# Performance work log

Hardware: AMD Instinct MI355X
Metric: run time of the kernel (lower is better)

The kernel has to match this reference:

```python
import jax, jax.numpy as jnp
import numpy as np

C = 1.0          # curvature of PoincareBall
SQRT_C = 1.0
MIN_NORM = 1e-15
PROJ_EPS = 4e-3  # float32 boundary eps used by PoincareBall.proj
N_NODES = 50000


def _norm(x):
    return jnp.clip(jnp.linalg.norm(x, axis=-1, keepdims=True), MIN_NORM)


def _artanh(x):
    return jnp.arctanh(jnp.clip(x, -1.0 + 1e-7, 1.0 - 1e-7))


def proj(x):
    # clip points to the open ball of radius (1-eps)/sqrt(c)
    norm = _norm(x)
    maxnorm = (1.0 - PROJ_EPS) / SQRT_C
    return jnp.where(norm > maxnorm, x / norm * maxnorm, x)


def expmap0(u):
    u_norm = _norm(u)
    return jnp.tanh(SQRT_C * u_norm) * u / (SQRT_C * u_norm)


def logmap0(p):
    p_norm = _norm(p)
    return _artanh(SQRT_C * p_norm) * p / (SQRT_C * p_norm)


def mobius_add(x, y):
    x2 = jnp.sum(x * x, -1, keepdims=True)
    y2 = jnp.sum(y * y, -1, keepdims=True)
    xy = jnp.sum(x * y, -1, keepdims=True)
    num = (1.0 + 2.0 * C * xy + C * y2) * x + (1.0 - C * x2) * y
    den = 1.0 + 2.0 * C * xy + C * C * x2 * y2
    return num / jnp.clip(den, MIN_NORM)


def mobius_matvec(m, x):
    x_norm = _norm(x)
    mx = x @ m.T  # [N, d_out]
    mx_norm = _norm(mx)
    res = jnp.tanh(mx_norm / x_norm * _artanh(SQRT_C * x_norm)) * mx / (mx_norm * SQRT_C)
    zero_row = jnp.all(mx == 0, axis=-1, keepdims=True)
    return jnp.where(zero_row, jnp.zeros_like(res), res)


def setup_inputs() -> dict:
    key = jax.random.key(0)
    k = jax.random.split(key, 6)
    n, d_in, d_out, n_edges = N_NODES, 256, 96, 800000
    # points on the Poincare ball
    x = proj(0.02 * jax.random.normal(k[0], (n, d_in), jnp.float32))
    weight = jax.random.normal(k[1], (d_out, d_in), jnp.float32) * (1.0 / np.sqrt(d_in)).astype(np.float32)
    bias = jax.random.normal(k[2], (d_out,), jnp.float32) * 0.01
    edge_row = jax.random.randint(k[3], (n_edges,), 0, n)
    edge_col = jax.random.randint(k[4], (n_edges,), 0, n)
    # normalized adjacency weights ~ 1/avg_degree
    edge_weight = jax.random.uniform(k[5], (n_edges,), jnp.float32) * (1.0 / 16.0)
    return {"x": x, "weight": weight, "bias": bias, "edge_weight": edge_weight,
            "edge_row": edge_row, "edge_col": edge_col}


def reference(x, weight, bias, edge_weight, edge_row, edge_col):
    # --- HypLinear (dropout inactive in eval) ---
    h = proj(mobius_matvec(weight, x))
    hyp_bias = proj(expmap0(bias[None, :]))  # proj_tan0 is identity on the ball
    h = proj(mobius_add(h, hyp_bias))
    # --- HypAgg: spmm(adj, logmap0(h)) then expmap0 ---
    xt = logmap0(h)                                  # [N, d_out]
    msgs = edge_weight[:, None] * xt[edge_col]       # [E, d_out]
    support = jax.ops.segment_sum(msgs, edge_row, num_segments=N_NODES)
    h = proj(expmap0(support))
    # --- HypAct: relu in tangent space, map back (c_in == c_out) ---
    h = proj(expmap0(jax.nn.relu(logmap0(h))))
    return h
```

## Files before the change

### kernel.cpp

```cpp
#include <hip/hip_runtime.h>


typedef __attribute__((ext_vector_type(8))) short short8;
typedef __attribute__((ext_vector_type(4))) float floatx4;

#define DIN 256
#define DOUT 96
#define MAXN 0.996f
#define EPS15 1e-15f
#define ATC (1.0f - 1e-7f)
#define STR 48

__device__ __forceinline__ float us2f(unsigned short u) {
    unsigned int v = ((unsigned int)u) << 16;
    return __uint_as_float(v);
}
__device__ __forceinline__ unsigned short f2us(float f) {
    unsigned int b = __float_as_uint(f);
    unsigned int r = (b + 0x7FFFu + ((b >> 16) & 1u)) >> 16;
    return (unsigned short)r;
}

__global__ void initzero_kernel(const unsigned short* __restrict__ xraw,
                                const void* __restrict__ bias,
                                const void* __restrict__ wgt,
                                float* __restrict__ ws,
                                int* __restrict__ deg, int N) {
    int i = blockIdx.x * blockDim.x + threadIdx.x;
    int stride = gridDim.x * blockDim.x;
    for (int k = i; k < N; k += stride) deg[k] = 0;

    if (blockIdx.x == 0 && threadIdx.x < 64) {
        int l = threadIdx.x;
        float v0 = us2f(xraw[l]);
        float v1 = us2f(xraw[64 + l]);
        int big = (!(fabsf(v0) < 1e4f)) || (!(fabsf(v1) < 1e4f));
        #pragma unroll
        for (int m = 32; m >= 1; m >>= 1) big |= __shfl_xor(big, m, 64);
        bool isb = !big;
        if (l == 0) ws[97] = isb ? 1.0f : 0.0f;

        float b0 = isb ? us2f(((const unsigned short*)bias)[l])
                       : ((const float*)bias)[l];
        float b1 = 0.0f;
        if (l < 32)
            b1 = isb ? us2f(((const unsigned short*)bias)[64 + l])
                     : ((const float*)bias)[64 + l];
        float n2 = b0 * b0 + b1 * b1;
        #pragma unroll
        for (int m = 32; m >= 1; m >>= 1) n2 += __shfl_xor(n2, m, 64);
        float bn = fmaxf(sqrtf(n2), EPS15);
        float ef = tanhf(bn) / bn;
        float hn = ef * sqrtf(n2);
        float s = (hn > MAXN) ? MAXN / fmaxf(hn, EPS15) : 1.0f;
        ws[l] = s * ef * b0;
        if (l < 32) ws[64 + l] = s * ef * b1;
        if (l == 0) { float v = s * hn; ws[96] = v * v; }
    }

    if (blockIdx.x == 1) {
        int t = threadIdx.x, lane = t & 63;
        float v0 = us2f(xraw[lane]);
        float v1 = us2f(xraw[64 + lane]);
        int big = (!(fabsf(v0) < 1e4f)) || (!(fabsf(v1) < 1e4f));
        #pragma unroll
        for (int m = 32; m >= 1; m >>= 1) big |= __shfl_xor(big, m, 64);
        bool isb = !big;
        uint4* wz = (uint4*)(ws + 128);
        if (isb) {
            const uint4* wg = (const uint4*)wgt;
            #pragma unroll
            for (int it = 0; it < 12; it++) {
                int g = t + 256 * it;
                int c = g >> 5, j = g & 31;
                int f = c >> 4, mr = c & 15;
                int kt = j >> 2, q = j & 3;
                wz[(f * 8 + kt) * 64 + q * 16 + mr] = wg[g];
            }
        } else {
            const float* wgf = (const float*)wgt;
            #pragma unroll
            for (int it = 0; it < 12; it++) {
                int g = t + 256 * it;
                int c = g >> 5, j = g & 31;
                int f = c >> 4, mr = c & 15;
                int kt = j >> 2, q = j & 3;
                const float* src = wgf + (size_t)c * DIN + j * 8;
                unsigned short tmp[8];
                #pragma unroll
                for (int z = 0; z < 8; z++) tmp[z] = f2us(src[z]);
                wz[(f * 8 + kt) * 64 + q * 16 + mr] = *(const uint4*)tmp;
            }
        }
    }
}

__global__ void fillhyp_kernel(const void* __restrict__ x,
                               const void* __restrict__ ew,
                               const int* __restrict__ erow,
                               const int* __restrict__ ecol,
                               float* __restrict__ ws,
                               unsigned int* __restrict__ einfo,
                               unsigned short* __restrict__ xtb,
                               int* __restrict__ deg,
                               int N, int E, int Fb) {
    const int t = threadIdx.x;
    const bool isb = ws[97] != 0.0f;

    int b = blockIdx.x;
    bool isfill; int idx;
    if (b < 2 * Fb) { isfill = (b & 1); idx = b >> 1; }
    else            { isfill = false;   idx = b - Fb; }

    if (isfill) {
        int stride = Fb * 256;
        for (int e = idx * 256 + t; e < E; e += stride) {
            unsigned int wbits = isb ? (unsigned int)((const unsigned short*)ew)[e]
                                     : (unsigned int)f2us(((const float*)ew)[e]);
            int row = erow[e];
            int p = atomicAdd(&deg[row], 1);
            if (p < STR)
                einfo[(size_t)row * STR + p] = (wbits << 16) | (unsigned int)ecol[e];
        }
        return;
    }

    const int lane = t & 63;
    const int wv = t >> 6;
    const int mrow = lane & 15;
    const int quad = lane >> 4;
    const uint4* __restrict__ Wg = (const uint4*)(ws + 128);

    const int r0 = (idx * 4 + wv) * 16;
    if (r0 >= N) return;

    float hbl[6];
    #pragma unroll
    for (int f = 0; f < 6; f++) hbl[f] = ws[mrow + 16 * f];
    const float hb2 = ws[96];

    int xr = r0 + mrow; if (xr >= N) xr = N - 1;
    short8 afrag[8];
    if (isb) {
        const unsigned short* xrow = (const unsigned short*)x + (size_t)xr * DIN + quad * 8;
        #pragma unroll
        for (int kt = 0; kt < 8; kt++)
            afrag[kt] = *(const short8*)(xrow + kt * 32);
    } else {
        const float* xrow = (const float*)x + (size_t)xr * DIN + quad * 8;
        #pragma unroll
        for (int kt = 0; kt < 8; kt++) {
            short8 a;
            #pragma unroll
            for (int j = 0; j < 8; j++) a[j] = (short)f2us(xrow[kt * 32 + j]);
            afrag[kt] = a;
        }
    }

    float xn2p = 0.f;
    #pragma unroll
    for (int kt = 0; kt < 8; kt++)
        #pragma unroll
        for (int j = 0; j < 8; j++) {
            float v = us2f((unsigned short)afrag[kt][j]);
            xn2p = fmaf(v, v, xn2p);
        }
    xn2p += __shfl_xor(xn2p, 16, 64);
    xn2p += __shfl_xor(xn2p, 32, 64);

    floatx4 acc[6];
    #pragma unroll
    for (int f = 0; f < 6; f++) acc[f] = (floatx4){0.f, 0.f, 0.f, 0.f};
    #pragma unroll
    for (int f = 0; f < 6; f++) {
        uint4 bw[8];
        #pragma unroll
        for (int kt = 0; kt < 8; kt++)
            bw[kt] = Wg[(f * 8 + kt) * 64 + lane];
        #pragma unroll
        for (int kt = 0; kt < 8; kt++) {
            short8 bfr = *(const short8*)&bw[kt];
            acc[f] = __builtin_amdgcn_mfma_f32_16x16x32_bf16(afrag[kt], bfr, acc[f], 0, 0, 0);
        }
    }

    float mxn2[4], dmh[4];
    #pragma unroll
    for (int reg = 0; reg < 4; reg++) {
        float a2 = 0.f, ad = 0.f;
        #pragma unroll
        for (int f = 0; f < 6; f++) {
            float v = acc[f][reg];
            a2 = fmaf(v, v, a2);
            ad = fmaf(v, hbl[f], ad);
        }
        mxn2[reg] = a2; dmh[reg] = ad;
    }
    #pragma unroll
    for (int m = 8; m >= 1; m >>= 1)
        #pragma unroll
        for (int reg = 0; reg < 4; reg++) {
            mxn2[reg] += __shfl_xor(mxn2[reg], m, 64);
            dmh[reg]  += __shfl_xor(dmh[reg],  m, 64);
        }

    int sel = mrow & 3;
    float xn2  = __shfl(xn2p, quad * 4 + sel, 64);
    float wmx2 = mxn2[sel], wdmh = dmh[sel];

    float xn  = fmaxf(sqrtf(xn2), EPS15);
    float mxn = fmaxf(sqrtf(wmx2), EPS15);
    float g   = (mxn / xn) * atanhf(fminf(xn, ATC));
    float tg  = tanhf(g);
    float rs0 = tg / mxn;
    float rn  = rs0 * sqrtf(wmx2);
    float s1  = (rn > MAXN) ? MAXN / fmaxf(rn, EPS15) : 1.0f;
    float al  = s1 * rs0;
    float x2  = al * al * wmx2;
    float xy  = al * wdmh;
    float cA  = 1.0f + 2.0f * xy + hb2;
    float cB  = 1.0f - x2;
    float den = fmaxf(1.0f + 2.0f * xy + x2 * hb2, EPS15);
    float p   = cA * al / den;
    float qq  = cB / den;
    float o2  = p*p*wmx2 + 2.0f*p*qq*wdmh + qq*qq*hb2;
    float on  = sqrtf(fmaxf(o2, 0.0f));
    float s2  = (on > MAXN) ? MAXN / fmaxf(on, EPS15) : 1.0f;
    float pn  = fmaxf(s2 * on, EPS15);
    float F   = (atanhf(fminf(pn, ATC)) / pn) * s2;
    float Fp_m = F * p, Fq_m = F * qq;

    float Fp[4], Fq[4];
    #pragma unroll
    for (int reg = 0; reg < 4; reg++) {
        Fp[reg] = __shfl(Fp_m, quad * 16 + reg, 64);
        Fq[reg] = __shfl(Fq_m, quad * 16 + reg, 64);
    }

    #pragma unroll
    for (int reg = 0; reg < 4; reg++) {
        int row = r0 + quad * 4 + reg;
        if (row < N) {
            size_t base = (size_t)row * DOUT + mrow;
            #pragma unroll
            for (int f = 0; f < 6; f++)
                xtb[base + 16 * f] = f2us(fmaf(Fp[reg], acc[f][reg], Fq[reg] * hbl[f]));
        }
    }
}

__global__ void agg_kernel(const unsigned short* __restrict__ xtb,
                           const unsigned int* __restrict__ einfo,
                           const int* __restrict__ deg,
                           float* __restrict__ ws,
                           void* __restrict__ out, int N) {
    int wv = threadIdx.x >> 6, lane = threadIdx.x & 63;
    int node = blockIdx.x * 4 + wv;
    if (node >= N) return;
    const bool isb = ws[97] != 0.0f;
    const bool act = lane < 48;

    int cnt = deg[node]; if (cnt > STR) cnt = STR;
    size_t base = (size_t)node * STR;
    float acc0 = 0.f, acc1 = 0.f;

    unsigned int my = (lane < cnt) ? einfo[base + lane] : 0u;

    int j = 0;
    for (; j + 8 <= cnt; j += 8) {
        float w[8]; const unsigned int* sp[8];
        #pragma unroll
        for (int k = 0; k < 8; k++) {
            unsigned int ei = (unsigned int)__shfl((int)my, j + k, 64);
            w[k] = __uint_as_float(ei & 0xFFFF0000u);
            sp[k] = (const unsigned int*)(xtb + (size_t)(ei & 0xFFFFu) * DOUT);
        }
        unsigned int u[8];
        #pragma unroll
        for (int k = 0; k < 8; k++) u[k] = act ? sp[k][lane] : 0u;
        #pragma unroll
        for (int k = 0; k < 8; k++) {
            acc0 = fmaf(w[k], __uint_as_float(u[k] << 16), acc0);
            acc1 = fmaf(w[k], __uint_as_float(u[k] & 0xFFFF0000u), acc1);
        }
    }
    for (; j < cnt; j++) {
        unsigned int ei = (unsigned int)__shfl((int)my, j, 64);
        float w = __uint_as_float(ei & 0xFFFF0000u);
        unsigned int u = act
            ? ((const unsigned int*)(xtb + (size_t)(ei & 0xFFFFu) * DOUT))[lane] : 0u;
        acc0 = fmaf(w, __uint_as_float(u << 16), acc0);
        acc1 = fmaf(w, __uint_as_float(u & 0xFFFF0000u), acc1);
    }

    float u0 = acc0, u1 = acc1;
    float n2 = u0*u0 + u1*u1;
    #pragma unroll
    for (int m = 32; m >= 1; m >>= 1) n2 += __shfl_xor(n2, m, 64);
    float un = fmaxf(sqrtf(n2), EPS15);
    float ef = tanhf(un) / un;
    float p0 = ef * u0, p1 = ef * u1;
    float pnrm = ef * sqrtf(n2);
    float sc = (pnrm > MAXN) ? MAXN / fmaxf(pnrm, EPS15) : 1.0f;
    p0 *= sc; p1 *= sc; pnrm *= sc;
    float pncl = fmaxf(pnrm, EPS15);
    float lf = atanhf(fminf(pncl, ATC)) / pncl;
    float t0 = fmaxf(lf * p0, 0.0f), t1 = fmaxf(lf * p1, 0.0f);
    float tn2 = t0*t0 + t1*t1;
    #pragma unroll
    for (int m = 32; m >= 1; m >>= 1) tn2 += __shfl_xor(tn2, m, 64);
    float tn = fmaxf(sqrtf(tn2), EPS15);
    float ef2 = tanhf(tn) / tn;
    float en = ef2 * sqrtf(tn2);
    float s2 = (en > MAXN) ? MAXN / fmaxf(en, EPS15) : 1.0f;
    float scale = s2 * ef2;
    float v0 = scale * t0, v1 = scale * t1;

    if (act) {
        if (isb) {
            unsigned int pk = ((unsigned int)f2us(v1) << 16) | (unsigned int)f2us(v0);
            ((unsigned int*)((unsigned short*)out + (size_t)node * DOUT))[lane] = pk;
        } else {
            float2 fv; fv.x = v0; fv.y = v1;
            ((float2*)((float*)out + (size_t)node * DOUT))[lane] = fv;
        }
    }
}

extern "C" void kernel_launch(void* const* d_in, const int* in_sizes, int n_in,
                              void* d_out, int out_size, void* d_ws, size_t ws_size,
                              hipStream_t stream) {
    const void* x    = d_in[0];
    const void* wgt  = d_in[1];
    const void* bias = d_in[2];
    const void* ew   = d_in[3];
    const int* erow  = (const int*)d_in[4];
    const int* ecol  = (const int*)d_in[5];

    int N = out_size / DOUT;
    int E = in_sizes[4];
    size_t nd = (size_t)N * DOUT;

    float* wsf = (float*)d_ws;
    unsigned int* einfo = (unsigned int*)(wsf + 128 + 12288);
    unsigned short* xtb = (unsigned short*)(einfo + (size_t)N * STR);
    int* deg            = (int*)(xtb + nd);

    int Hb = (N + 63) / 64;
    int Fb = (Hb + 1) / 2;

    initzero_kernel<<<128, 256, 0, stream>>>((const unsigned short*)x, bias, wgt, wsf, deg, N);
    fillhyp_kernel<<<Hb + Fb, 256, 0, stream>>>(x, ew, erow, ecol, wsf,
                                                einfo, xtb, deg, N, E, Fb);
    agg_kernel<<<(N + 3) / 4, 256, 0, stream>>>(xtb, einfo, deg, wsf, d_out, N);
}
```

Baseline: 190.7 us.

## Pad degree counters, batch fill atomics, double-buffer gathers, parallelize weight repack

Degree counters are spread to one per 64-byte stride when workspace allows, to cut atomic contention and false sharing between rows. The edge-fill loop now handles four edges per thread, issuing all loads before the atomics so more memory requests are in flight. The aggregation gather is double-buffered so the next 8 neighbor loads are issued before the current batch is accumulated. Weight repacking is split across 12 blocks instead of one. The padded counters raise zero-init traffic and workspace use, and the unrolled aggregation raises register pressure.

```diff
diff --git a/kernel.cpp b/kernel.cpp
--- a/kernel.cpp
+++ b/kernel.cpp
@@ -25,10 +25,11 @@
                                 const void* __restrict__ bias,
                                 const void* __restrict__ wgt,
                                 float* __restrict__ ws,
-                                int* __restrict__ deg, int N) {
+                                int* __restrict__ deg, int N, int dstr) {
     int i = blockIdx.x * blockDim.x + threadIdx.x;
     int stride = gridDim.x * blockDim.x;
-    for (int k = i; k < N; k += stride) deg[k] = 0;
+    int tot = N * dstr;
+    for (int k = i; k < tot; k += stride) deg[k] = 0;
 
     if (blockIdx.x == 0 && threadIdx.x < 64) {
         int l = threadIdx.x;
@@ -58,7 +59,7 @@
         if (l == 0) { float v = s * hn; ws[96] = v * v; }
     }
 
-    if (blockIdx.x == 1) {
+    if (blockIdx.x >= 1 && blockIdx.x <= 12) {
         int t = threadIdx.x, lane = t & 63;
         float v0 = us2f(xraw[lane]);
         float v1 = us2f(xraw[64 + lane]);
@@ -67,30 +68,20 @@
         for (int m = 32; m >= 1; m >>= 1) big |= __shfl_xor(big, m, 64);
         bool isb = !big;
         uint4* wz = (uint4*)(ws + 128);
+        int g = t + 256 * (int)(blockIdx.x - 1);
+        int c = g >> 5, j = g & 31;
+        int f = c >> 4, mr = c & 15;
+        int kt = j >> 2, q = j & 3;
         if (isb) {
             const uint4* wg = (const uint4*)wgt;
-            #pragma unroll
-            for (int it = 0; it < 12; it++) {
-                int g = t + 256 * it;
-                int c = g >> 5, j = g & 31;
-                int f = c >> 4, mr = c & 15;
-                int kt = j >> 2, q = j & 3;
-                wz[(f * 8 + kt) * 64 + q * 16 + mr] = wg[g];
-            }
+            wz[(f * 8 + kt) * 64 + q * 16 + mr] = wg[g];
         } else {
             const float* wgf = (const float*)wgt;
-            #pragma unroll
-            for (int it = 0; it < 12; it++) {
-                int g = t + 256 * it;
-                int c = g >> 5, j = g & 31;
-                int f = c >> 4, mr = c & 15;
-                int kt = j >> 2, q = j & 3;
-                const float* src = wgf + (size_t)c * DIN + j * 8;
-                unsigned short tmp[8];
-                #pragma unroll
-                for (int z = 0; z < 8; z++) tmp[z] = f2us(src[z]);
-                wz[(f * 8 + kt) * 64 + q * 16 + mr] = *(const uint4*)tmp;
-            }
+            const float* src = wgf + (size_t)c * DIN + j * 8;
+            unsigned short tmp[8];
+            #pragma unroll
+            for (int z = 0; z < 8; z++) tmp[z] = f2us(src[z]);
+            wz[(f * 8 + kt) * 64 + q * 16 + mr] = *(const uint4*)tmp;
         }
     }
 }
@@ -103,7 +94,7 @@
                                unsigned int* __restrict__ einfo,
                                unsigned short* __restrict__ xtb,
                                int* __restrict__ deg,
-                               int N, int E, int Fb) {
+                               int N, int E, int Fb, int dstr) {
     const int t = threadIdx.x;
     const bool isb = ws[97] != 0.0f;
 
@@ -113,14 +104,29 @@
     else            { isfill = false;   idx = b - Fb; }
 
     if (isfill) {
-        int stride = Fb * 256;
-        for (int e = idx * 256 + t; e < E; e += stride) {
-            unsigned int wbits = isb ? (unsigned int)((const unsigned short*)ew)[e]
-                                     : (unsigned int)f2us(((const float*)ew)[e]);
-            int row = erow[e];
-            int p = atomicAdd(&deg[row], 1);
-            if (p < STR)
-                einfo[(size_t)row * STR + p] = (wbits << 16) | (unsigned int)ecol[e];
+        const int T4 = Fb * 1024;
+        for (int e0 = idx * 1024 + t; e0 < E; e0 += T4) {
+            int row[4], col[4]; unsigned int wb[4]; bool va[4];
+            #pragma unroll
+            for (int u = 0; u < 4; u++) {
+                int e = e0 + 256 * u;
+                va[u] = e < E;
+                if (va[u]) {
+                    wb[u] = isb ? (unsigned int)((const unsigned short*)ew)[e]
+                                : (unsigned int)f2us(((const float*)ew)[e]);
+                    row[u] = erow[e];
+                    col[u] = ecol[e];
+                }
+            }
+            int p[4];
+            #pragma unroll
+            for (int u = 0; u < 4; u++)
+                if (va[u]) p[u] = atomicAdd(&deg[row[u] * dstr], 1);
+            #pragma unroll
+            for (int u = 0; u < 4; u++)
+                if (va[u] && p[u] < STR)
+                    einfo[(size_t)row[u] * STR + p[u]] =
+                        (wb[u] << 16) | (unsigned int)col[u];
         }
         return;
     }
@@ -253,45 +259,63 @@
                            const unsigned int* __restrict__ einfo,
                            const int* __restrict__ deg,
                            float* __restrict__ ws,
-                           void* __restrict__ out, int N) {
+                           void* __restrict__ out, int N, int dstr) {
     int wv = threadIdx.x >> 6, lane = threadIdx.x & 63;
     int node = blockIdx.x * 4 + wv;
     if (node >= N) return;
     const bool isb = ws[97] != 0.0f;
     const bool act = lane < 48;
 
-    int cnt = deg[node]; if (cnt > STR) cnt = STR;
+    int cnt = deg[(size_t)node * dstr]; if (cnt > STR) cnt = STR;
     size_t base = (size_t)node * STR;
     float acc0 = 0.f, acc1 = 0.f;
 
     unsigned int my = (lane < cnt) ? einfo[base + lane] : 0u;
 
-    int j = 0;
-    for (; j + 8 <= cnt; j += 8) {
-        float w[8]; const unsigned int* sp[8];
-        #pragma unroll
-        for (int k = 0; k < 8; k++) {
-            unsigned int ei = (unsigned int)__shfl((int)my, j + k, 64);
-            w[k] = __uint_as_float(ei & 0xFFFF0000u);
-            sp[k] = (const unsigned int*)(xtb + (size_t)(ei & 0xFFFFu) * DOUT);
-        }
-        unsigned int u[8];
-        #pragma unroll
-        for (int k = 0; k < 8; k++) u[k] = act ? sp[k][lane] : 0u;
-        #pragma unroll
-        for (int k = 0; k < 8; k++) {
-            acc0 = fmaf(w[k], __uint_as_float(u[k] << 16), acc0);
-            acc1 = fmaf(w[k], __uint_as_float(u[k] & 0xFFFF0000u), acc1);
-        }
-    }
-    for (; j < cnt; j++) {
-        unsigned int ei = (unsigned int)__shfl((int)my, j, 64);
-        float w = __uint_as_float(ei & 0xFFFF0000u);
-        unsigned int u = act
-            ? ((const unsigned int*)(xtb + (size_t)(ei & 0xFFFFu) * DOUT))[lane] : 0u;
-        acc0 = fmaf(w, __uint_as_float(u << 16), acc0);
-        acc1 = fmaf(w, __uint_as_float(u & 0xFFFF0000u), acc1);
-    }
+    unsigned int uA[8], uB[8];
+    float wA[8], wB[8];
+
+#define ISSUE(BU, BW, B)                                                       \
+    _Pragma("unroll")                                                          \
+    for (int k = 0; k < 8; k++) {                                              \
+        unsigned int ei = (unsigned int)__shfl((int)my, (B) * 8 + k, 64);      \
+        BW[k] = __uint_as_float(ei & 0xFFFF0000u);                             \
+        const unsigned int* sp =                                               \
+            (const unsigned int*)(xtb + (size_t)(ei & 0xFFFFu) * DOUT);        \
+        BU[k] = (act && ((B) * 8 + k) < cnt) ? sp[lane] : 0u;                  \
+    }
+
+#define CONSUME(BU, BW)                                                        \
+    _Pragma("unroll")                                                          \
+    for (int k = 0; k < 8; k++) {                                              \
+        acc0 = fmaf(BW[k], __uint_as_float(BU[k] << 16), acc0);                \
+        acc1 = fmaf(BW[k], __uint_as_float(BU[k] & 0xFFFF0000u), acc1);        \
+    }
+
+    if (cnt > 0) {
+        ISSUE(uA, wA, 0);
+        if (cnt > 8) ISSUE(uB, wB, 1);
+        CONSUME(uA, wA);
+        if (cnt > 8) {
+            if (cnt > 16) ISSUE(uA, wA, 2);
+            CONSUME(uB, wB);
+            if (cnt > 16) {
+                if (cnt > 24) ISSUE(uB, wB, 3);
+                CONSUME(uA, wA);
+                if (cnt > 24) {
+                    if (cnt > 32) ISSUE(uA, wA, 4);
+                    CONSUME(uB, wB);
+                    if (cnt > 32) {
+                        if (cnt > 40) ISSUE(uB, wB, 5);
+                        CONSUME(uA, wA);
+                        if (cnt > 40) CONSUME(uB, wB);
+                    }
+                }
+            }
+        }
+    }
+#undef ISSUE
+#undef CONSUME
 
     float u0 = acc0, u1 = acc1;
     float n2 = u0*u0 + u1*u1;
@@ -346,11 +370,14 @@
     unsigned short* xtb = (unsigned short*)(einfo + (size_t)N * STR);
     int* deg            = (int*)(xtb + nd);
 
+    size_t fixed_bytes = ((size_t)(128 + 12288) + (size_t)N * STR) * 4 + nd * 2;
+    int dstr = (ws_size >= fixed_bytes + (size_t)N * 16 * 4) ? 16 : 1;
+
     int Hb = (N + 63) / 64;
     int Fb = (Hb + 1) / 2;
 
-    initzero_kernel<<<128, 256, 0, stream>>>((const unsigned short*)x, bias, wgt, wsf, deg, N);
+    initzero_kernel<<<128, 256, 0, stream>>>((const unsigned short*)x, bias, wgt, wsf, deg, N, dstr);
     fillhyp_kernel<<<Hb + Fb, 256, 0, stream>>>(x, ew, erow, ecol, wsf,
-                                                einfo, xtb, deg, N, E, Fb);
-    agg_kernel<<<(N + 3) / 4, 256, 0, stream>>>(xtb, einfo, deg, wsf, d_out, N);
-}
+                                                einfo, xtb, deg, N, E, Fb, dstr);
+    agg_kernel<<<(N + 3) / 4, 256, 0, stream>>>(xtb, einfo, deg, wsf, d_out, N, dstr);
+}
```

After: 182.2 us. -4.5%, faster.

## Replace per-node atomic edge lists with block-bucketed partition and LDS-atomic aggregation

Applied to the files above, without the earlier changes.

Edges are now bucketed by row block (128 rows per bucket) through a tiled partition kernel. It builds a local histogram and prefix sum in shared memory, then reserves one global atomic per bucket, which replaces the per-edge global atomics on node degree counters. Aggregation runs one block per bucket and accumulates messages into a 128x96 shared-memory tile with LDS atomics, using double-buffered gathers. The hyperbolic linear stage is split into its own kernel, and the weight repacking is spread over 12 blocks. This changes the per-node cap of 48 edges to a per-bucket cap of 2560 and hardcodes the bucket count to the problem size. It also adds heavy shared-atomic contention and low parallelism in aggregation, since there are only 391 blocks.

```diff
diff --git a/kernel.cpp b/kernel.cpp
--- a/kernel.cpp
+++ b/kernel.cpp
@@ -9,7 +9,9 @@
 #define MAXN 0.996f
 #define EPS15 1e-15f
 #define ATC (1.0f - 1e-7f)
-#define STR 48
+#define NBK 391
+#define CAP 2560
+#define TILE 6144
 
 __device__ __forceinline__ float us2f(unsigned short u) {
     unsigned int v = ((unsigned int)u) << 16;
@@ -25,10 +27,10 @@
                                 const void* __restrict__ bias,
                                 const void* __restrict__ wgt,
                                 float* __restrict__ ws,
-                                int* __restrict__ deg, int N) {
+                                int* __restrict__ gcur) {
     int i = blockIdx.x * blockDim.x + threadIdx.x;
     int stride = gridDim.x * blockDim.x;
-    for (int k = i; k < N; k += stride) deg[k] = 0;
+    for (int k = i; k < NBK * 16; k += stride) gcur[k] = 0;
 
     if (blockIdx.x == 0 && threadIdx.x < 64) {
         int l = threadIdx.x;
@@ -58,7 +60,7 @@
         if (l == 0) { float v = s * hn; ws[96] = v * v; }
     }
 
-    if (blockIdx.x == 1) {
+    if (blockIdx.x >= 1 && blockIdx.x <= 12) {
         int t = threadIdx.x, lane = t & 63;
         float v0 = us2f(xraw[lane]);
         float v1 = us2f(xraw[64 + lane]);
@@ -67,71 +69,115 @@
         for (int m = 32; m >= 1; m >>= 1) big |= __shfl_xor(big, m, 64);
         bool isb = !big;
         uint4* wz = (uint4*)(ws + 128);
+        int g = t + 256 * (int)(blockIdx.x - 1);
+        int c = g >> 5, j = g & 31;
+        int f = c >> 4, mr = c & 15;
+        int kt = j >> 2, q = j & 3;
         if (isb) {
             const uint4* wg = (const uint4*)wgt;
-            #pragma unroll
-            for (int it = 0; it < 12; it++) {
-                int g = t + 256 * it;
-                int c = g >> 5, j = g & 31;
-                int f = c >> 4, mr = c & 15;
-                int kt = j >> 2, q = j & 3;
-                wz[(f * 8 + kt) * 64 + q * 16 + mr] = wg[g];
-            }
+            wz[(f * 8 + kt) * 64 + q * 16 + mr] = wg[g];
         } else {
             const float* wgf = (const float*)wgt;
+            const float* src = wgf + (size_t)c * DIN + j * 8;
+            unsigned short tmp[8];
             #pragma unroll
-            for (int it = 0; it < 12; it++) {
-                int g = t + 256 * it;
-                int c = g >> 5, j = g & 31;
-                int f = c >> 4, mr = c & 15;
-                int kt = j >> 2, q = j & 3;
-                const float* src = wgf + (size_t)c * DIN + j * 8;
-                unsigned short tmp[8];
-                #pragma unroll
-                for (int z = 0; z < 8; z++) tmp[z] = f2us(src[z]);
-                wz[(f * 8 + kt) * 64 + q * 16 + mr] = *(const uint4*)tmp;
-            }
-        }
-    }
-}
-
-__global__ void fillhyp_kernel(const void* __restrict__ x,
-                               const void* __restrict__ ew,
-                               const int* __restrict__ erow,
-                               const int* __restrict__ ecol,
-                               float* __restrict__ ws,
-                               unsigned int* __restrict__ einfo,
-                               unsigned short* __restrict__ xtb,
-                               int* __restrict__ deg,
-                               int N, int E, int Fb) {
+            for (int z = 0; z < 8; z++) tmp[z] = f2us(src[z]);
+            wz[(f * 8 + kt) * 64 + q * 16 + mr] = *(const uint4*)tmp;
+        }
+    }
+}
+
+__global__ void __launch_bounds__(256) part_kernel(
+        const void* __restrict__ ew,
+        const int* __restrict__ erow,
+        const int* __restrict__ ecol,
+        const float* __restrict__ ws,
+        int* __restrict__ gcur,
+        uint2* __restrict__ arena, int E) {
+    __shared__ uint2 stage[TILE];
+    __shared__ int h[NBK], excl[NBK], cur[NBK], gb[NBK];
+    __shared__ int cb[64];
+
     const int t = threadIdx.x;
     const bool isb = ws[97] != 0.0f;
-
-    int b = blockIdx.x;
-    bool isfill; int idx;
-    if (b < 2 * Fb) { isfill = (b & 1); idx = b >> 1; }
-    else            { isfill = false;   idx = b - Fb; }
-
-    if (isfill) {
-        int stride = Fb * 256;
-        for (int e = idx * 256 + t; e < E; e += stride) {
-            unsigned int wbits = isb ? (unsigned int)((const unsigned short*)ew)[e]
-                                     : (unsigned int)f2us(((const float*)ew)[e]);
-            int row = erow[e];
-            int p = atomicAdd(&deg[row], 1);
-            if (p < STR)
-                einfo[(size_t)row * STR + p] = (wbits << 16) | (unsigned int)ecol[e];
-        }
-        return;
-    }
-
+    const int tb = blockIdx.x * TILE;
+    const int tcnt = min(TILE, E - tb);
+
+    for (int i = t; i < NBK; i += 256) h[i] = 0;
+    __syncthreads();
+
+    int rw[24]; unsigned int pk[24];
+    #pragma unroll
+    for (int k = 0; k < 24; k++) {
+        int e = tb + t + 256 * k;
+        if (e < E) {
+            int r = erow[e];
+            unsigned int wb = isb ? (unsigned int)((const unsigned short*)ew)[e]
+                                  : (unsigned int)f2us(((const float*)ew)[e]);
+            rw[k] = r;
+            pk[k] = (wb << 16) | (unsigned int)ecol[e];
+            atomicAdd(&h[r >> 7], 1);
+        } else rw[k] = -1;
+    }
+    __syncthreads();
+
+    if (t < 64) {
+        int s = 0;
+        #pragma unroll
+        for (int j = 0; j < 8; j++) {
+            int b2 = t * 8 + j;
+            if (b2 < NBK) s += h[b2];
+        }
+        int sc = s;
+        #pragma unroll
+        for (int d = 1; d < 64; d <<= 1) {
+            int tt = __shfl_up(sc, d, 64);
+            if (t >= d) sc += tt;
+        }
+        cb[t] = sc - s;
+    }
+    __syncthreads();
+    for (int b2 = t; b2 < NBK; b2 += 256) {
+        int base = cb[b2 >> 3];
+        int x = 0;
+        for (int j = (b2 & ~7); j < b2; j++) x += h[j];
+        excl[b2] = base + x;
+        cur[b2]  = base + x;
+        gb[b2] = atomicAdd(&gcur[b2 * 16], h[b2]);
+    }
+    __syncthreads();
+
+    #pragma unroll
+    for (int k = 0; k < 24; k++) {
+        if (rw[k] >= 0) {
+            int b2 = rw[k] >> 7;
+            int slot = atomicAdd(&cur[b2], 1);
+            stage[slot] = make_uint2(pk[k], (unsigned int)rw[k]);
+        }
+    }
+    __syncthreads();
+
+    for (int s = t; s < tcnt; s += 256) {
+        uint2 ent = stage[s];
+        int b2 = (int)ent.y >> 7;
+        int p = gb[b2] + (s - excl[b2]);
+        if (p < CAP) arena[(size_t)b2 * CAP + p] = ent;
+    }
+}
+
+__global__ void hyp_kernel(const void* __restrict__ x,
+                           float* __restrict__ ws,
+                           unsigned short* __restrict__ xtb,
+                           int N) {
+    const int t = threadIdx.x;
+    const bool isb = ws[97] != 0.0f;
     const int lane = t & 63;
     const int wv = t >> 6;
     const int mrow = lane & 15;
     const int quad = lane >> 4;
     const uint4* __restrict__ Wg = (const uint4*)(ws + 128);
 
-    const int r0 = (idx * 4 + wv) * 16;
+    const int r0 = ((int)blockIdx.x * 4 + wv) * 16;
     if (r0 >= N) return;
 
     float hbl[6];
@@ -249,80 +295,109 @@
     }
 }
 
-__global__ void agg_kernel(const unsigned short* __restrict__ xtb,
-                           const unsigned int* __restrict__ einfo,
-                           const int* __restrict__ deg,
-                           float* __restrict__ ws,
-                           void* __restrict__ out, int N) {
-    int wv = threadIdx.x >> 6, lane = threadIdx.x & 63;
-    int node = blockIdx.x * 4 + wv;
-    if (node >= N) return;
+__global__ void __launch_bounds__(512) agg_kernel(
+        const unsigned short* __restrict__ xtb,
+        const uint2* __restrict__ arena,
+        const int* __restrict__ gcur,
+        const float* __restrict__ ws,
+        void* __restrict__ out, int N) {
+    __shared__ float acc[128 * 96];
+
+    const int t = threadIdx.x;
+    const int lane = t & 63, wv = t >> 6;
+    const int b = blockIdx.x;
     const bool isb = ws[97] != 0.0f;
-    const bool act = lane < 48;
-
-    int cnt = deg[node]; if (cnt > STR) cnt = STR;
-    size_t base = (size_t)node * STR;
-    float acc0 = 0.f, acc1 = 0.f;
-
-    unsigned int my = (lane < cnt) ? einfo[base + lane] : 0u;
-
-    int j = 0;
-    for (; j + 8 <= cnt; j += 8) {
-        float w[8]; const unsigned int* sp[8];
-        #pragma unroll
-        for (int k = 0; k < 8; k++) {
-            unsigned int ei = (unsigned int)__shfl((int)my, j + k, 64);
-            w[k] = __uint_as_float(ei & 0xFFFF0000u);
-            sp[k] = (const unsigned int*)(xtb + (size_t)(ei & 0xFFFFu) * DOUT);
-        }
-        unsigned int u[8];
-        #pragma unroll
-        for (int k = 0; k < 8; k++) u[k] = act ? sp[k][lane] : 0u;
-        #pragma unroll
-        for (int k = 0; k < 8; k++) {
-            acc0 = fmaf(w[k], __uint_as_float(u[k] << 16), acc0);
-            acc1 = fmaf(w[k], __uint_as_float(u[k] & 0xFFFF0000u), acc1);
-        }
-    }
-    for (; j < cnt; j++) {
-        unsigned int ei = (unsigned int)__shfl((int)my, j, 64);
-        float w = __uint_as_float(ei & 0xFFFF0000u);
-        unsigned int u = act
-            ? ((const unsigned int*)(xtb + (size_t)(ei & 0xFFFFu) * DOUT))[lane] : 0u;
-        acc0 = fmaf(w, __uint_as_float(u << 16), acc0);
-        acc1 = fmaf(w, __uint_as_float(u & 0xFFFF0000u), acc1);
-    }
-
-    float u0 = acc0, u1 = acc1;
-    float n2 = u0*u0 + u1*u1;
-    #pragma unroll
-    for (int m = 32; m >= 1; m >>= 1) n2 += __shfl_xor(n2, m, 64);
-    float un = fmaxf(sqrtf(n2), EPS15);
-    float ef = tanhf(un) / un;
-    float p0 = ef * u0, p1 = ef * u1;
-    float pnrm = ef * sqrtf(n2);
-    float sc = (pnrm > MAXN) ? MAXN / fmaxf(pnrm, EPS15) : 1.0f;
-    p0 *= sc; p1 *= sc; pnrm *= sc;
-    float pncl = fmaxf(pnrm, EPS15);
-    float lf = atanhf(fminf(pncl, ATC)) / pncl;
-    float t0 = fmaxf(lf * p0, 0.0f), t1 = fmaxf(lf * p1, 0.0f);
-    float tn2 = t0*t0 + t1*t1;
-    #pragma unroll
-    for (int m = 32; m >= 1; m >>= 1) tn2 += __shfl_xor(tn2, m, 64);
-    float tn = fmaxf(sqrtf(tn2), EPS15);
-    float ef2 = tanhf(tn) / tn;
-    float en = ef2 * sqrtf(tn2);
-    float s2 = (en > MAXN) ? MAXN / fmaxf(en, EPS15) : 1.0f;
-    float scale = s2 * ef2;
-    float v0 = scale * t0, v1 = scale * t1;
-
-    if (act) {
-        if (isb) {
-            unsigned int pk = ((unsigned int)f2us(v1) << 16) | (unsigned int)f2us(v0);
-            ((unsigned int*)((unsigned short*)out + (size_t)node * DOUT))[lane] = pk;
-        } else {
-            float2 fv; fv.x = v0; fv.y = v1;
-            ((float2*)((float*)out + (size_t)node * DOUT))[lane] = fv;
+
+    for (int i = t; i < 128 * 96; i += 512) acc[i] = 0.0f;
+    __syncthreads();
+
+    int cnt = gcur[b * 16]; if (cnt > CAP) cnt = CAP;
+    const size_t abase = (size_t)b * CAP;
+
+    unsigned int uA[8], uB[8];
+    float wA[8], wB[8];
+    int rA[8], rB[8];
+
+#define AGG_ISSUE(U, W, R, BB)                                              \
+    _Pragma("unroll")                                                       \
+    for (int k = 0; k < 8; k++) {                                           \
+        int idx = (BB) * 8 + k;                                             \
+        unsigned int ex = (unsigned int)__shfl((int)my.x, idx, 64);         \
+        unsigned int ey = (unsigned int)__shfl((int)my.y, idx, 64);         \
+        bool v = idx < navail;                                              \
+        W[k] = __uint_as_float(ex & 0xFFFF0000u);                           \
+        R[k] = v ? (int)(ey & 127u) : -1;                                   \
+        const unsigned int* sp =                                            \
+            (const unsigned int*)(xtb + (size_t)(ex & 0xFFFFu) * DOUT);     \
+        U[k] = (v && lane < 48) ? sp[lane] : 0u;                            \
+    }
+
+#define AGG_CONSUME(U, W, R)                                                \
+    _Pragma("unroll")                                                       \
+    for (int k = 0; k < 8; k++) {                                           \
+        if (R[k] >= 0 && lane < 48) {                                       \
+            atomicAdd(&acc[R[k] * 96 + 2 * lane],                           \
+                      W[k] * __uint_as_float(U[k] << 16));                  \
+            atomicAdd(&acc[R[k] * 96 + 2 * lane + 1],                       \
+                      W[k] * __uint_as_float(U[k] & 0xFFFF0000u));          \
+        }                                                                   \
+    }
+
+    for (int cs = wv * 64; cs < cnt; cs += 512) {
+        int navail = cnt - cs; if (navail > 64) navail = 64;
+        uint2 my = (lane < navail) ? arena[abase + cs + lane]
+                                   : make_uint2(0u, 0u);
+        int nb = (navail + 7) >> 3;
+        AGG_ISSUE(uA, wA, rA, 0);
+        for (int bb = 1; bb < nb; bb++) {
+            if (bb & 1) { AGG_ISSUE(uB, wB, rB, bb); AGG_CONSUME(uA, wA, rA); }
+            else        { AGG_ISSUE(uA, wA, rA, bb); AGG_CONSUME(uB, wB, rB); }
+        }
+        if (nb & 1) { AGG_CONSUME(uA, wA, rA); }
+        else        { AGG_CONSUME(uB, wB, rB); }
+    }
+#undef AGG_ISSUE
+#undef AGG_CONSUME
+    __syncthreads();
+
+    for (int r8 = 0; r8 < 16; r8++) {
+        int row = wv + 8 * r8;
+        int rg = b * 128 + row;
+        float a0 = 0.f, a1 = 0.f;
+        if (lane < 48) {
+            a0 = acc[row * 96 + 2 * lane];
+            a1 = acc[row * 96 + 2 * lane + 1];
+        }
+        float n2 = a0*a0 + a1*a1;
+        #pragma unroll
+        for (int m = 32; m >= 1; m >>= 1) n2 += __shfl_xor(n2, m, 64);
+        float un = fmaxf(sqrtf(n2), EPS15);
+        float ef = tanhf(un) / un;
+        float p0 = ef * a0, p1 = ef * a1;
+        float pnrm = ef * sqrtf(n2);
+        float sc = (pnrm > MAXN) ? MAXN / fmaxf(pnrm, EPS15) : 1.0f;
+        p0 *= sc; p1 *= sc; pnrm *= sc;
+        float pncl = fmaxf(pnrm, EPS15);
+        float lf = atanhf(fminf(pncl, ATC)) / pncl;
+        float t0 = fmaxf(lf * p0, 0.0f), t1 = fmaxf(lf * p1, 0.0f);
+        float tn2 = t0*t0 + t1*t1;
+        #pragma unroll
+        for (int m = 32; m >= 1; m >>= 1) tn2 += __shfl_xor(tn2, m, 64);
+        float tn = fmaxf(sqrtf(tn2), EPS15);
+        float ef2 = tanhf(tn) / tn;
+        float en = ef2 * sqrtf(tn2);
+        float s2 = (en > MAXN) ? MAXN / fmaxf(en, EPS15) : 1.0f;
+        float scale = s2 * ef2;
+        float v0 = scale * t0, v1 = scale * t1;
+
+        if (rg < N && lane < 48) {
+            if (isb) {
+                unsigned int pkv = ((unsigned int)f2us(v1) << 16) | (unsigned int)f2us(v0);
+                ((unsigned int*)((unsigned short*)out + (size_t)rg * DOUT))[lane] = pkv;
+            } else {
+                float2 fv; fv.x = v0; fv.y = v1;
+                ((float2*)((float*)out + (size_t)rg * DOUT))[lane] = fv;
+            }
         }
     }
 }
@@ -339,18 +414,17 @@
 
     int N = out_size / DOUT;
     int E = in_sizes[4];
-    size_t nd = (size_t)N * DOUT;
 
     float* wsf = (float*)d_ws;
-    unsigned int* einfo = (unsigned int*)(wsf + 128 + 12288);
-    unsigned short* xtb = (unsigned short*)(einfo + (size_t)N * STR);
-    int* deg            = (int*)(xtb + nd);
-
+    int* gcur = (int*)(wsf + 128 + 12288);
+    uint2* arena = (uint2*)((char*)d_ws + 74688);
+    unsigned short* xtb = (unsigned short*)((char*)d_ws + 74688 + (size_t)NBK * CAP * 8);
+
+    int Pb = (E + TILE - 1) / TILE;
     int Hb = (N + 63) / 64;
-    int Fb = (Hb + 1) / 2;
-
-    initzero_kernel<<<128, 256, 0, stream>>>((const unsigned short*)x, bias, wgt, wsf, deg, N);
-    fillhyp_kernel<<<Hb + Fb, 256, 0, stream>>>(x, ew, erow, ecol, wsf,
-                                                einfo, xtb, deg, N, E, Fb);
-    agg_kernel<<<(N + 3) / 4, 256, 0, stream>>>(xtb, einfo, deg, wsf, d_out, N);
-}
+
+    initzero_kernel<<<13, 256, 0, stream>>>((const unsigned short*)x, bias, wgt, wsf, gcur);
+    part_kernel<<<Pb, 256, 0, stream>>>(ew, erow, ecol, wsf, gcur, arena, E);
+    hyp_kernel<<<Hb, 256, 0, stream>>>(x, wsf, xtb, N);
+    agg_kernel<<<NBK, 512, 0, stream>>>(xtb, arena, gcur, wsf, d_out, N);
+}
```

New measurement: 700.7 us. 267% more time.
